# Performance work log

Hardware: AMD Instinct MI355X
Metric: run time of the kernel (lower is better)

## Reference

```python
import jax, jax.numpy as jnp
import numpy as np

B, C, L = 32, 64, 2048
FREQ = L // 2 + 1            # 1025
BAND_SIZES = [341, 341, 343]  # freq//3, freq//3, remainder


def setup_inputs() -> dict:
    key = jax.random.key(0)
    k = jax.random.split(key, 6)
    X = jax.random.normal(k[0], (B, C, L), dtype=jnp.float32)
    A0 = jax.random.normal(k[1], (BAND_SIZES[0], BAND_SIZES[0]), dtype=jnp.float32)
    A1 = jax.random.normal(k[2], (BAND_SIZES[1], BAND_SIZES[1]), dtype=jnp.float32)
    A2 = jax.random.normal(k[3], (BAND_SIZES[2], BAND_SIZES[2]), dtype=jnp.float32)
    fusion_weights = jnp.ones((3,), dtype=jnp.float32)
    # Gumbel(0,1) noise for the 2-way gumbel-softmax over each (b, i, j) entry
    gumbel_noise = jax.random.gumbel(k[4], (B, C, C, 2), dtype=jnp.float32)
    return {"X": X, "A0": A0, "A1": A1, "A2": A2,
            "fusion_weights": fusion_weights, "gumbel_noise": gumbel_noise}


def _band_dist(band, A):
    # band: (b, c, s), A: (s, s). dist[b,i,j] = ||A (band_i - band_j)||^2
    # Gram trick: ||y_i - y_j||^2 = q_i + q_j - 2 y_i . y_j, y = band @ A^T
    Y = jnp.einsum('ds,bcs->bcd', A, band)          # (b, c, s)
    G = jnp.einsum('bid,bjd->bij', Y, Y)            # (b, c, c)
    q = jnp.einsum('bid,bid->bi', Y, Y)             # (b, c)
    dist = q[:, :, None] + q[:, None, :] - 2.0 * G
    return jnp.maximum(dist, 0.0)                   # guard fp round-off


def reference(X, A0, A1, A2, fusion_weights, gumbel_noise):
    XF = jnp.abs(jnp.fft.rfft(X, axis=-1))          # (b, c, FREQ)
    s0, s1, s2 = BAND_SIZES
    bands = (XF[..., :s0], XF[..., s0:s0 + s1], XF[..., s0 + s1:])
    As = (A0, A1, A2)
    dists = jnp.stack([_band_dist(b_, A_) for b_, A_ in zip(bands, As)], axis=-1)  # (b,c,c,3)
    w = jax.nn.softmax(fusion_weights)
    dist = jnp.einsum('bijk,k->bij', dists, w)      # (b, c, c)

    exp_dist = 1.0 / (dist + 1e-10)
    eye = jnp.eye(C, dtype=exp_dist.dtype)
    mask = 1.0 - eye
    exp_dist = exp_dist * mask
    exp_max = jax.lax.stop_gradient(jnp.max(exp_dist, axis=-1, keepdims=True))
    p = exp_dist / exp_max
    p = (p * mask + eye) * 0.99                     # probs in (0, 0.99]

    # Bernoulli via 2-class gumbel-softmax (hard, tau=1, straight-through)
    logits = jnp.stack([jnp.log(p / (1.0 - p)), jnp.log((1.0 - p) / p)], axis=-1)  # (b,c,c,2)
    y = logits + gumbel_noise
    y_soft = jax.nn.softmax(y, axis=-1)
    y_hard = jax.nn.one_hot(jnp.argmax(y, axis=-1), 2, dtype=y_soft.dtype)
    sample = (y_hard - jax.lax.stop_gradient(y_soft) + y_soft)[..., 0]  # (b,c,c)
    return sample[:, None, :, :]                    # (b, 1, c, c)
```

## Files before the change

### kernel.cpp

```cpp
#include <hip/hip_runtime.h>
#include <math.h>

#define Bn 32
#define Cn 64
#define Ln 2048
#define NFREQ 1025
#define S0c 341
#define S1c 341
#define S2c 343

#define PI_D 3.14159265358979323846

typedef double v4d __attribute__((ext_vector_type(4)));

#define PADIX(i) ((i) + ((i) >> 4))

__global__ void k_twiddle(double2* __restrict__ tw) {
    int t = blockIdx.x * blockDim.x + threadIdx.x;
    if (t < 2048) {
        double ang = -2.0 * PI_D * (double)t / 2048.0;
        double s, c;
        sincos(ang, &s, &c);
        tw[t] = make_double2(c, s);
    }
}

__device__ __forceinline__ int rev4_10(unsigned x) {
    unsigned t = __brev(x) >> 22;
    return (int)(((t & 0x155u) << 1) | ((t >> 1) & 0x155u));
}

__global__ __launch_bounds__(256) void k_fft(const float* __restrict__ X,
                                             const double2* __restrict__ tw,
                                             float* __restrict__ XF) {
    __shared__ double re[2][1088];
    __shared__ double im[2][1088];
    int row0 = blockIdx.x * 2;
    int tid = threadIdx.x;
    {
        int k = tid;
        double2 w1 = tw[2 * k];
        double2 w2 = tw[4 * k];
        double2 w3 = tw[6 * k];
        int i0 = PADIX(k), i1 = PADIX(k + 256), i2 = PADIX(k + 512), i3 = PADIX(k + 768);
        #pragma unroll
        for (int r = 0; r < 2; ++r) {
            const float2* xr = (const float2*)(X + (size_t)(row0 + r) * Ln);
            float2 v0 = xr[k];
            float2 v1 = xr[k + 256];
            float2 v2 = xr[k + 512];
            float2 v3 = xr[k + 768];
            double ar = (double)v0.x, ai = (double)v0.y;
            double br = (double)v1.x, bi = (double)v1.y;
            double cr = (double)v2.x, ci = (double)v2.y;
            double dr = (double)v3.x, di = (double)v3.y;
            double t0r = ar + cr, t0i = ai + ci;
            double t1r = ar - cr, t1i = ai - ci;
            double t2r = br + dr, t2i = bi + di;
            double t3r = br - dr, t3i = bi - di;
            re[r][i0] = t0r + t2r; im[r][i0] = t0i + t2i;
            double u1r = t1r + t3i, u1i = t1i - t3r;
            re[r][i1] = u1r * w1.x - u1i * w1.y; im[r][i1] = u1r * w1.y + u1i * w1.x;
            double u2r = t0r - t2r, u2i = t0i - t2i;
            re[r][i2] = u2r * w2.x - u2i * w2.y; im[r][i2] = u2r * w2.y + u2i * w2.x;
            double u3r = t1r - t3i, u3i = t1i + t3r;
            re[r][i3] = u3r * w3.x - u3i * w3.y; im[r][i3] = u3r * w3.y + u3i * w3.x;
        }
    }
    __syncthreads();
    #pragma unroll
    for (int s = 1; s < 5; ++s) {
        int log2Q = 8 - 2 * s;
        int Q = 1 << log2Q;
        int k = tid & (Q - 1);
        int g = tid >> log2Q;
        int base = (g << (log2Q + 2)) + k;
        int i0 = PADIX(base), i1 = PADIX(base + Q), i2 = PADIX(base + 2 * Q), i3 = PADIX(base + 3 * Q);
        int step = 2 << (2 * s);
        double2 w1 = tw[k * step];
        double2 w2 = tw[2 * k * step];
        double2 w3 = tw[3 * k * step];
        #pragma unroll
        for (int r = 0; r < 2; ++r) {
            double ar = re[r][i0], ai = im[r][i0];
            double br = re[r][i1], bi = im[r][i1];
            double cr = re[r][i2], ci = im[r][i2];
            double dr = re[r][i3], di = im[r][i3];
            double t0r = ar + cr, t0i = ai + ci;
            double t1r = ar - cr, t1i = ai - ci;
            double t2r = br + dr, t2i = bi + di;
            double t3r = br - dr, t3i = bi - di;
            re[r][i0] = t0r + t2r; im[r][i0] = t0i + t2i;
            double u1r = t1r + t3i, u1i = t1i - t3r;
            re[r][i1] = u1r * w1.x - u1i * w1.y; im[r][i1] = u1r * w1.y + u1i * w1.x;
            double u2r = t0r - t2r, u2i = t0i - t2i;
            re[r][i2] = u2r * w2.x - u2i * w2.y; im[r][i2] = u2r * w2.y + u2i * w2.x;
            double u3r = t1r - t3i, u3i = t1i + t3r;
            re[r][i3] = u3r * w3.x - u3i * w3.y; im[r][i3] = u3r * w3.y + u3i * w3.x;
        }
        __syncthreads();
    }
    float* out0 = XF + (size_t)row0 * NFREQ;
    float* out1 = XF + (size_t)(row0 + 1) * NFREQ;
    for (int k = tid; k <= 1024; k += 256) {
        int rv = 0, rv2 = 0;
        double2 t = tw[0];
        if (k != 0 && k != 1024) {
            rv  = PADIX(rev4_10((unsigned)k));
            rv2 = PADIX(rev4_10((unsigned)(1024 - k)));
            t = tw[k];
        }
        #pragma unroll
        for (int r = 0; r < 2; ++r) {
            double Xr, Xi;
            if (k == 0)        { Xr = re[r][0] + im[r][0]; Xi = 0.0; }
            else if (k == 1024){ Xr = re[r][0] - im[r][0]; Xi = 0.0; }
            else {
                double Zr = re[r][rv],  Zi = im[r][rv];
                double Wr = re[r][rv2], Wi = im[r][rv2];
                double Er = 0.5 * (Zr + Wr), Ei = 0.5 * (Zi - Wi);
                double Or = 0.5 * (Zi + Wi), Oi = -0.5 * (Zr - Wr);
                Xr = Er + t.x * Or - t.y * Oi;
                Xi = Ei + t.x * Oi + t.y * Or;
            }
            float v = (float)sqrt(Xr * Xr + Xi * Xi);
            if (r == 0) out0[k] = v; else out1[k] = v;
        }
    }
}

__global__ __launch_bounds__(256) void k_gemm(const float* __restrict__ XF,
                                              const float* __restrict__ A0,
                                              const float* __restrict__ A1,
                                              const float* __restrict__ A2,
                                              double* __restrict__ Y) {
    const int Sarr[3] = {S0c, S1c, S2c};
    const int Oarr[3] = {0, S0c, S0c + S1c};
    int bz = blockIdx.z;
    int z = bz >> 2, q = bz & 3;
    const float* A = (z == 0) ? A0 : ((z == 1) ? A1 : A2);
    int S = Sarr[z], O = Oarr[z];
    int qm = q >> 1, qn = q & 1;

    __shared__ float sX[32][34];
    __shared__ float sA[32][34];
    int r0 = blockIdx.x * 64 + qm * 32;
    int d0 = blockIdx.y * 64 + qn * 32;
    int tid = threadIdx.x;
    int lane = tid & 63, w = tid >> 6;
    int lm = (w >> 1) * 16, ln = (w & 1) * 16;
    int fm = lane & 15, kq = lane >> 4;
    int kl = tid & 31, rl = tid >> 5;

    v4d zero = {0.0, 0.0, 0.0, 0.0};
    double aval = (double)fm;
    v4d calR = __builtin_amdgcn_mfma_f64_16x16x4f64(aval, 1.0, zero, 0, 0, 0);
    v4d calC = __builtin_amdgcn_mfma_f64_16x16x4f64(1.0, aval, zero, 0, 0, 0);
    int rIdx[4], cIdx[4];
    #pragma unroll
    for (int i = 0; i < 4; ++i) {
        rIdx[i] = (int)(calR[i] * 0.25);
        cIdx[i] = (int)(calC[i] * 0.25);
    }

    auto load_tile = [&](int st, float* px, float* pa) {
        int ss = st * 32 + kl;
        bool sv = ss < S;
        #pragma unroll
        for (int i = 0; i < 4; ++i)
            px[i] = sv ? XF[(size_t)(r0 + rl + 8 * i) * NFREQ + O + ss] : 0.0f;
        #pragma unroll
        for (int j = 0; j < 4; ++j) {
            int d = d0 + rl + 8 * j;
            pa[j] = (sv && d < S) ? A[(size_t)d * S + ss] : 0.0f;
        }
    };

    v4d acc = zero;
    float px[4], pa[4];
    load_tile(0, px, pa);
    int nsteps = (S + 31) / 32;
    for (int st = 0; st < nsteps; ++st) {
        __syncthreads();
        #pragma unroll
        for (int i = 0; i < 4; ++i) sX[rl + 8 * i][kl] = px[i];
        #pragma unroll
        for (int j = 0; j < 4; ++j) sA[rl + 8 * j][kl] = pa[j];
        __syncthreads();
        if (st + 1 < nsteps) load_tile(st + 1, px, pa);
        #pragma unroll
        for (int t = 0; t < 8; ++t) {
            int k = 4 * t + kq;
            double a = (double)sX[lm + fm][k];
            double b = (double)sA[ln + fm][k];
            acc = __builtin_amdgcn_mfma_f64_16x16x4f64(a, b, acc, 0, 0, 0);
        }
    }
    #pragma unroll
    for (int i = 0; i < 4; ++i) {
        int row = r0 + lm + rIdx[i];
        int d = d0 + ln + cIdx[i];
        if (d < S) Y[(size_t)row * NFREQ + O + d] = acc[i];
    }
}

__global__ __launch_bounds__(256) void k_dist(const double* __restrict__ Y,
                                              const float* __restrict__ fw,
                                              double* __restrict__ part) {
    __shared__ double sY[64][34];
    int b = blockIdx.x;
    int chunk = blockIdx.y;
    int dlo = chunk * 128;
    int dhi = (chunk == 7) ? NFREQ : dlo + 128;
    int tid = threadIdx.x;
    int lane = tid & 63, w = tid >> 6;
    int wm = (w >> 1) * 32, wn = (w & 1) * 32;
    int fm = lane & 15, kq = lane >> 4;
    int kl = tid & 31, rl = tid >> 5;

    double f0 = (double)fw[0], f1 = (double)fw[1], f2 = (double)fw[2];
    double m = fmax(f0, fmax(f1, f2));
    double e0 = exp(f0 - m), e1 = exp(f1 - m), e2 = exp(f2 - m);
    double esum = e0 + e1 + e2;
    double sw0 = sqrt(e0 / esum), sw1 = sqrt(e1 / esum), sw2 = sqrt(e2 / esum);

    v4d zero = {0.0, 0.0, 0.0, 0.0};
    double aval = (double)fm;
    v4d calR = __builtin_amdgcn_mfma_f64_16x16x4f64(aval, 1.0, zero, 0, 0, 0);
    v4d calC = __builtin_amdgcn_mfma_f64_16x16x4f64(1.0, aval, zero, 0, 0, 0);
    int rIdx[4], cIdx[4];
    #pragma unroll
    for (int i = 0; i < 4; ++i) {
        rIdx[i] = (int)(calR[i] * 0.25);
        cIdx[i] = (int)(calC[i] * 0.25);
    }

    const double* Yb = Y + (size_t)b * Cn * NFREQ;
    auto load_tile = [&](int k0, double* py) {
        int d = dlo + k0 + kl;
        bool dv = d < dhi;
        double sw = dv ? ((d < S0c) ? sw0 : ((d < S0c + S1c) ? sw1 : sw2)) : 0.0;
        #pragma unroll
        for (int i = 0; i < 8; ++i)
            py[i] = dv ? Yb[(size_t)(rl + 8 * i) * NFREQ + d] * sw : 0.0;
    };

    v4d acc00 = zero, acc01 = zero, acc10 = zero, acc11 = zero;
    double py[8];
    load_tile(0, py);
    int nsteps = (dhi - dlo + 31) / 32;
    for (int st = 0; st < nsteps; ++st) {
        __syncthreads();
        #pragma unroll
        for (int i = 0; i < 8; ++i) sY[rl + 8 * i][kl] = py[i];
        __syncthreads();
        if (st + 1 < nsteps) load_tile((st + 1) * 32, py);
        #pragma unroll
        for (int t = 0; t < 8; ++t) {
            int k = 4 * t + kq;
            double a0 = sY[wm + fm][k];
            double a1 = sY[wm + 16 + fm][k];
            double b0 = sY[wn + fm][k];
            double b1 = sY[wn + 16 + fm][k];
            acc00 = __builtin_amdgcn_mfma_f64_16x16x4f64(a0, b0, acc00, 0, 0, 0);
            acc01 = __builtin_amdgcn_mfma_f64_16x16x4f64(a0, b1, acc01, 0, 0, 0);
            acc10 = __builtin_amdgcn_mfma_f64_16x16x4f64(a1, b0, acc10, 0, 0, 0);
            acc11 = __builtin_amdgcn_mfma_f64_16x16x4f64(a1, b1, acc11, 0, 0, 0);
        }
    }
    double* pb = part + (((size_t)b * 8 + chunk) << 12);
    #pragma unroll
    for (int i = 0; i < 4; ++i) {
        int rowA = wm + rIdx[i], rowB = rowA + 16;
        int cA = wn + cIdx[i], cB = cA + 16;
        pb[rowA * 64 + cA] = acc00[i];
        pb[rowA * 64 + cB] = acc01[i];
        pb[rowB * 64 + cA] = acc10[i];
        pb[rowB * 64 + cB] = acc11[i];
    }
}

__global__ __launch_bounds__(256) void k_decide(const double* __restrict__ part,
                                                const float* __restrict__ gum,
                                                float* __restrict__ out) {
    __shared__ double sQ[64];
    int b = blockIdx.x;
    int tid = threadIdx.x;
    const double* pb = part + (((size_t)b * 8) << 12);
    if (tid < 64) {
        double q = 0.0;
        #pragma unroll
        for (int c = 0; c < 8; ++c) q += pb[((size_t)c << 12) + tid * 65];
        sQ[tid] = q;
    }
    __syncthreads();
    int i = blockIdx.y * 4 + (tid >> 6);
    int j = tid & 63;
    double g = 0.0;
    #pragma unroll
    for (int c = 0; c < 8; ++c) g += pb[((size_t)c << 12) + i * 64 + j];
    double dist = fmax(sQ[i] + sQ[j] - 2.0 * g, 0.0);
    double e = (i == j) ? 0.0 : 1.0 / (dist + 1e-10);
    double emax = e;
    #pragma unroll
    for (int off = 32; off; off >>= 1)
        emax = fmax(emax, __shfl_xor(emax, off, 64));
    double p = (i == j) ? 0.99 : (e / emax) * 0.99;
    double l0 = log(p / (1.0 - p));
    double l1 = log((1.0 - p) / p);
    int idx = i * 64 + j;
    const float* gb = gum + (size_t)b * 8192;
    double y0 = l0 + (double)gb[2 * idx];
    double y1 = l1 + (double)gb[2 * idx + 1];
    out[(size_t)b * 4096 + idx] = (y0 >= y1) ? 1.0f : 0.0f;
}

extern "C" void kernel_launch(void* const* d_in, const int* in_sizes, int n_in,
                              void* d_out, int out_size, void* d_ws, size_t ws_size,
                              hipStream_t stream) {
    const float* X  = (const float*)d_in[0];
    const float* A0 = (const float*)d_in[1];
    const float* A1 = (const float*)d_in[2];
    const float* A2 = (const float*)d_in[3];
    const float* fw = (const float*)d_in[4];
    const float* gm = (const float*)d_in[5];
    float* out = (float*)d_out;

    char* ws = (char*)d_ws;
    double2* tw  = (double2*)(ws);
    float*   XF  = (float*)(ws + 32768);
    double*  Y   = (double*)(ws + 8429568);
    double*  part = (double*)(ws + 32768);

    k_twiddle<<<8, 256, 0, stream>>>(tw);
    k_fft<<<Bn * Cn / 2, 256, 0, stream>>>(X, tw, XF);
    k_gemm<<<dim3(32, 6, 12), 256, 0, stream>>>(XF, A0, A1, A2, Y);
    k_dist<<<dim3(Bn, 8), 256, 0, stream>>>(Y, fw, part);
    k_decide<<<dim3(Bn, 16), 256, 0, stream>>>(part, gm, out);
}
```

Before: 162.5 us.

## Enlarge GEMM block tile to 128x32 with 2x2 MFMA register tiling per wave

Restructures the band GEMM so each block computes a 128-row by 32-column tile, and each wave computes a 32x32 sub-tile using four f64 MFMA accumulators. This reuses each loaded A and B fragment twice and cuts the total block count from 2304 to 528. The goal is fewer redundant shared-memory and global loads per MFMA. The cost is more registers per thread (16 prefetch floats plus four accumulators) and fewer blocks, which may leave the GPU under-occupied.

```diff
diff --git a/kernel.cpp b/kernel.cpp
--- a/kernel.cpp
+++ b/kernel.cpp
@@ -136,19 +136,17 @@
                                               double* __restrict__ Y) {
     const int Sarr[3] = {S0c, S1c, S2c};
     const int Oarr[3] = {0, S0c, S0c + S1c};
-    int bz = blockIdx.z;
-    int z = bz >> 2, q = bz & 3;
+    int z = blockIdx.z;
     const float* A = (z == 0) ? A0 : ((z == 1) ? A1 : A2);
     int S = Sarr[z], O = Oarr[z];
-    int qm = q >> 1, qn = q & 1;
-
-    __shared__ float sX[32][34];
+
+    __shared__ float sX[128][34];
     __shared__ float sA[32][34];
-    int r0 = blockIdx.x * 64 + qm * 32;
-    int d0 = blockIdx.y * 64 + qn * 32;
+    int r0 = blockIdx.x * 128;
+    int d0 = blockIdx.y * 32;
     int tid = threadIdx.x;
     int lane = tid & 63, w = tid >> 6;
-    int lm = (w >> 1) * 16, ln = (w & 1) * 16;
+    int wr = w * 32;
     int fm = lane & 15, kq = lane >> 4;
     int kl = tid & 31, rl = tid >> 5;
 
@@ -167,7 +165,7 @@
         int ss = st * 32 + kl;
         bool sv = ss < S;
         #pragma unroll
-        for (int i = 0; i < 4; ++i)
+        for (int i = 0; i < 16; ++i)
             px[i] = sv ? XF[(size_t)(r0 + rl + 8 * i) * NFREQ + O + ss] : 0.0f;
         #pragma unroll
         for (int j = 0; j < 4; ++j) {
@@ -176,14 +174,14 @@
         }
     };
 
-    v4d acc = zero;
-    float px[4], pa[4];
+    v4d acc00 = zero, acc01 = zero, acc10 = zero, acc11 = zero;
+    float px[16], pa[4];
     load_tile(0, px, pa);
     int nsteps = (S + 31) / 32;
     for (int st = 0; st < nsteps; ++st) {
         __syncthreads();
         #pragma unroll
-        for (int i = 0; i < 4; ++i) sX[rl + 8 * i][kl] = px[i];
+        for (int i = 0; i < 16; ++i) sX[rl + 8 * i][kl] = px[i];
         #pragma unroll
         for (int j = 0; j < 4; ++j) sA[rl + 8 * j][kl] = pa[j];
         __syncthreads();
@@ -191,16 +189,30 @@
         #pragma unroll
         for (int t = 0; t < 8; ++t) {
             int k = 4 * t + kq;
-            double a = (double)sX[lm + fm][k];
-            double b = (double)sA[ln + fm][k];
-            acc = __builtin_amdgcn_mfma_f64_16x16x4f64(a, b, acc, 0, 0, 0);
+            double a0 = (double)sX[wr + fm][k];
+            double a1 = (double)sX[wr + 16 + fm][k];
+            double b0 = (double)sA[fm][k];
+            double b1 = (double)sA[16 + fm][k];
+            acc00 = __builtin_amdgcn_mfma_f64_16x16x4f64(a0, b0, acc00, 0, 0, 0);
+            acc01 = __builtin_amdgcn_mfma_f64_16x16x4f64(a0, b1, acc01, 0, 0, 0);
+            acc10 = __builtin_amdgcn_mfma_f64_16x16x4f64(a1, b0, acc10, 0, 0, 0);
+            acc11 = __builtin_amdgcn_mfma_f64_16x16x4f64(a1, b1, acc11, 0, 0, 0);
         }
     }
     #pragma unroll
     for (int i = 0; i < 4; ++i) {
-        int row = r0 + lm + rIdx[i];
-        int d = d0 + ln + cIdx[i];
-        if (d < S) Y[(size_t)row * NFREQ + O + d] = acc[i];
+        int ra = r0 + wr + rIdx[i];
+        int rb = ra + 16;
+        int ca = d0 + cIdx[i];
+        int cb = ca + 16;
+        if (ca < S) {
+            Y[(size_t)ra * NFREQ + O + ca] = acc00[i];
+            Y[(size_t)rb * NFREQ + O + ca] = acc10[i];
+        }
+        if (cb < S) {
+            Y[(size_t)ra * NFREQ + O + cb] = acc01[i];
+            Y[(size_t)rb * NFREQ + O + cb] = acc11[i];
+        }
     }
 }
 
@@ -334,7 +346,7 @@
 
     k_twiddle<<<8, 256, 0, stream>>>(tw);
     k_fft<<<Bn * Cn / 2, 256, 0, stream>>>(X, tw, XF);
-    k_gemm<<<dim3(32, 6, 12), 256, 0, stream>>>(XF, A0, A1, A2, Y);
+    k_gemm<<<dim3(16, 11, 3), 256, 0, stream>>>(XF, A0, A1, A2, Y);
     k_dist<<<dim3(Bn, 8), 256, 0, stream>>>(Y, fw, part);
     k_decide<<<dim3(Bn, 16), 256, 0, stream>>>(part, gm, out);
 }
```

After: 179.9 us. 10.7% more time.
